# Kernel optimization log

Measured on AMD Instinct MI355X. Metric: run time of the kernel, lower is better.

## Reference

```python
import jax, jax.numpy as jnp
import numpy as np
from jax import lax

NUM_TAGS = 48
BATCH = 512
SEQ_LEN = 1024


def setup_inputs() -> dict:
    key = jax.random.key(0)
    k1, k2, k3, k4 = jax.random.split(key, 4)
    emissions = jax.random.normal(k1, (BATCH, SEQ_LEN, NUM_TAGS), dtype=jnp.float32)
    mask = jnp.ones((BATCH, SEQ_LEN), dtype=jnp.int32)
    transitions = jax.random.normal(k2, (NUM_TAGS, NUM_TAGS), dtype=jnp.float32)
    start_transitions = jax.random.normal(k3, (NUM_TAGS,), dtype=jnp.float32)
    end_transitions = jax.random.normal(k4, (NUM_TAGS,), dtype=jnp.float32)
    return {
        "emissions": emissions,
        "mask": mask,
        "transitions": transitions,
        "start_transitions": start_transitions,
        "end_transitions": end_transitions,
    }


def reference(emissions, mask, transitions, start_transitions, end_transitions):
    """Viterbi decode. mask is accepted but unused, matching the original module."""
    # emissions: [B, S, T]
    init_scores = start_transitions + emissions[:, 0]  # [B, T]

    def step(scores, em_t):
        # scores: [B, T] best score ending in each prev tag
        scores_with_trans = scores[:, :, None] + transitions  # [B, Tprev, Tcur]
        idx = jnp.argmax(scores_with_trans, axis=1)            # [B, T] backpointers
        new_scores = jnp.max(scores_with_trans, axis=1) + em_t  # [B, T]
        return new_scores, idx

    # scan over timesteps 1..S-1 (time-major emissions)
    em_rest = jnp.swapaxes(emissions[:, 1:], 0, 1)  # [S-1, B, T]
    scores, backptrs = lax.scan(step, init_scores, em_rest)  # backptrs: [S-1, B, T]

    scores = scores + end_transitions
    best_tags = jnp.argmax(scores, axis=1)  # [B] tag at position S-1

    def backtrace(tag, bp_t):
        # tag: [B] tag at position t+1; bp_t: [B, T] backpointers into position t
        prev = jnp.take_along_axis(bp_t, tag[:, None], axis=1)[:, 0]
        return prev, tag  # emit tag at position t+1

    first_tag, tags_rest = lax.scan(backtrace, best_tags, backptrs, reverse=True)
    # tags_rest[i] = tag at position i+1, shape [S-1, B]
    best_paths = jnp.concatenate(
        [first_tag[:, None], jnp.swapaxes(tags_rest, 0, 1)], axis=1
    )  # [B, S]
    return best_paths
```

## Files before the change

kernel.cpp:

```cpp
#include <hip/hip_runtime.h>

#define NTAG 48
#define SEQ 1024
#define NBATCH 512
#define NEG_INF (-3.402823466e+38f)

__device__ __forceinline__ float rl_f32(float v, int lane) {
    return __int_as_float(__builtin_amdgcn_readlane(__float_as_int(v), lane));
}

__device__ __forceinline__ float max3(float a, float b, float c) {
    float d;
    asm("v_max3_f32 %0, %1, %2, %3" : "=v"(d) : "v"(a), "v"(b), "v"(c));
    return d;
}

__global__ __launch_bounds__(64, 1) void crf_viterbi_kernel(
    const float* __restrict__ em,
    const float* __restrict__ trans,
    const float* __restrict__ start,
    const float* __restrict__ endt,
    int* __restrict__ out,
    float* __restrict__ srows)
{
    const int b  = blockIdx.x;
    const int j  = threadIdx.x;
    const int jj = (j < NTAG) ? j : (NTAG - 1);

    __shared__ float Ttr[NTAG * NTAG];
    __shared__ int obuf[SEQ];

#pragma unroll
    for (int k = 0; k < (NTAG * NTAG + 63) / 64; ++k) {
        int idx = k * 64 + j;
        if (idx < NTAG * NTAG) {
            int i = idx / NTAG, c = idx % NTAG;
            Ttr[c * NTAG + i] = trans[idx];
        }
    }

    float trg[NTAG];
#pragma unroll
    for (int i = 0; i < NTAG; ++i) trg[i] = trans[i * NTAG + jj];

    const float* emb = em + (size_t)b * SEQ * NTAG;
    float* srb = srows + (size_t)b * SEQ * NTAG;

    float score = start[jj] + emb[jj];
    if (j < NTAG) srb[j] = score;

    float em_p1 = emb[1 * NTAG + jj];
    float em_p2 = emb[2 * NTAG + jj];

    for (int t = 1; t < SEQ; ++t) {
        float em_j = em_p1;
        em_p1 = em_p2;
        int tn = (t + 2 < SEQ) ? (t + 2) : (SEQ - 1);
        em_p2 = emb[tn * NTAG + jj];

        float l1[16];
#pragma unroll
        for (int k = 0; k < 16; ++k) {
            float c0 = rl_f32(score, 3 * k)     + trg[3 * k];
            float c1 = rl_f32(score, 3 * k + 1) + trg[3 * k + 1];
            float c2 = rl_f32(score, 3 * k + 2) + trg[3 * k + 2];
            l1[k] = max3(c0, c1, c2);
        }
        float l2[6];
        l2[0] = max3(l1[0],  l1[1],  l1[2]);
        l2[1] = max3(l1[3],  l1[4],  l1[5]);
        l2[2] = max3(l1[6],  l1[7],  l1[8]);
        l2[3] = max3(l1[9],  l1[10], l1[11]);
        l2[4] = max3(l1[12], l1[13], l1[14]);
        l2[5] = l1[15];
        float m0 = max3(l2[0], l2[1], l2[2]);
        float m1 = max3(l2[3], l2[4], l2[5]);
        float best = fmaxf(m0, m1);

        score = best + em_j;
        if (j < NTAG) srb[(size_t)t * NTAG + j] = score;
    }

    float fs = (j < NTAG) ? (score + endt[jj]) : NEG_INF;
    float mx = fs;
    mx = fmaxf(mx, __shfl_xor(mx, 32, 64));
    mx = fmaxf(mx, __shfl_xor(mx, 16, 64));
    mx = fmaxf(mx, __shfl_xor(mx,  8, 64));
    mx = fmaxf(mx, __shfl_xor(mx,  4, 64));
    mx = fmaxf(mx, __shfl_xor(mx,  2, 64));
    mx = fmaxf(mx, __shfl_xor(mx,  1, 64));
    unsigned long long bl = __ballot(fs == mx);
    int jt = __ffsll(bl) - 1;

    if (j == 0) obuf[SEQ - 1] = jt;
    __syncthreads();

    float cur[8], nxt[8];
    int r = SEQ - 2;
#pragma unroll
    for (int k = 0; k < 8; ++k)
        cur[k] = srb[(size_t)(r - k) * NTAG + jj];

    int t = SEQ - 1;
    while (t >= 1) {
        int n = (t >= 8) ? 8 : t;
        int r2 = r - 8;
#pragma unroll
        for (int k = 0; k < 8; ++k)
            if (r2 - k >= 0) nxt[k] = srb[(size_t)(r2 - k) * NTAG + jj];

#pragma unroll
        for (int k = 0; k < 8; ++k) {
            if (k < n) {
                float tv = Ttr[jt * NTAG + jj];
                float v  = (j < NTAG) ? (cur[k] + tv) : NEG_INF;
                float m  = v;
                m = fmaxf(m, __shfl_xor(m, 32, 64));
                m = fmaxf(m, __shfl_xor(m, 16, 64));
                m = fmaxf(m, __shfl_xor(m,  8, 64));
                m = fmaxf(m, __shfl_xor(m,  4, 64));
                m = fmaxf(m, __shfl_xor(m,  2, 64));
                m = fmaxf(m, __shfl_xor(m,  1, 64));
                unsigned long long b2 = __ballot(v == m);
                jt = __ffsll(b2) - 1;
                if (j == 0) obuf[t - 1 - k] = jt;
            }
        }
        t -= n; r -= 8;
#pragma unroll
        for (int k = 0; k < 8; ++k) cur[k] = nxt[k];
    }

    __syncthreads();

    int* outb = out + (size_t)b * SEQ;
#pragma unroll
    for (int t0 = 0; t0 < SEQ / 64; ++t0)
        outb[t0 * 64 + j] = obuf[t0 * 64 + j];
}

extern "C" void kernel_launch(void* const* d_in, const int* in_sizes, int n_in,
                              void* d_out, int out_size, void* d_ws, size_t ws_size,
                              hipStream_t stream) {
    const float* em    = (const float*)d_in[0];
    const float* trans = (const float*)d_in[2];
    const float* start = (const float*)d_in[3];
    const float* endt  = (const float*)d_in[4];
    int* out = (int*)d_out;
    float* srows = (float*)d_ws;

    crf_viterbi_kernel<<<NBATCH, 64, 0, stream>>>(em, trans, start, endt, out, srows);
}
```

Before: 973.4 us.

## Stage emissions and score rows through double-buffered LDS via async global_load_lds

Emissions for 128-step chunks are copied into a double-buffered LDS stage with global_load_lds, replacing per-step global register prefetch in the forward pass. The backtrace likewise streams saved score rows from workspace into LDS chunks instead of per-row register prefetch. The aim is to take global memory latency off the serial per-step critical path. In exchange it adds 48KB of LDS and full vmcnt waits per chunk. The backtrace also reads rows just written by global stores, which relies on memory ordering for those stores.

```diff
diff --git a/kernel.cpp b/kernel.cpp
--- a/kernel.cpp
+++ b/kernel.cpp
@@ -3,6 +3,10 @@
 #define NTAG 48
 #define SEQ 1024
 #define NBATCH 512
+#define CH 128
+#define NCH (SEQ / CH)
+#define CHF (CH * NTAG)
+#define NISS (CHF * 4 / 1024)
 #define NEG_INF (-3.402823466e+38f)
 
 __device__ __forceinline__ float rl_f32(float v, int lane) {
@@ -14,6 +18,11 @@
     asm("v_max3_f32 %0, %1, %2, %3" : "=v"(d) : "v"(a), "v"(b), "v"(c));
     return d;
 }
+
+#define GLDS16(gp, lp)                                                                   \
+    __builtin_amdgcn_global_load_lds((const __attribute__((address_space(1))) void*)(gp),\
+                                     (__attribute__((address_space(3))) void*)(lp),      \
+                                     16, 0, 0)
 
 __global__ __launch_bounds__(64, 1) void crf_viterbi_kernel(
     const float* __restrict__ em,
@@ -27,6 +36,7 @@
     const int j  = threadIdx.x;
     const int jj = (j < NTAG) ? j : (NTAG - 1);
 
+    __shared__ float stage[2][CHF];
     __shared__ float Ttr[NTAG * NTAG];
     __shared__ int obuf[SEQ];
 
@@ -46,39 +56,51 @@
     const float* emb = em + (size_t)b * SEQ * NTAG;
     float* srb = srows + (size_t)b * SEQ * NTAG;
 
-    float score = start[jj] + emb[jj];
+#pragma unroll
+    for (int k = 0; k < NISS; ++k)
+        GLDS16(emb + k * 256 + j * 4, &stage[0][k * 256]);
+    asm volatile("s_waitcnt vmcnt(0)" ::: "memory");
+
+    float score = start[jj] + stage[0][jj];
     if (j < NTAG) srb[j] = score;
 
-    float em_p1 = emb[1 * NTAG + jj];
-    float em_p2 = emb[2 * NTAG + jj];
+    int cb = 0;
+    for (int c = 0; c < NCH; ++c) {
+        if (c + 1 < NCH) {
+            const float* gs = emb + (size_t)(c + 1) * CHF;
+#pragma unroll
+            for (int k = 0; k < NISS; ++k)
+                GLDS16(gs + k * 256 + j * 4, &stage[cb ^ 1][k * 256]);
+        }
+        const int tt0 = (c == 0) ? 1 : 0;
+        for (int tt = tt0; tt < CH; ++tt) {
+            float em_j = stage[cb][tt * NTAG + jj];
 
-    for (int t = 1; t < SEQ; ++t) {
-        float em_j = em_p1;
-        em_p1 = em_p2;
-        int tn = (t + 2 < SEQ) ? (t + 2) : (SEQ - 1);
-        em_p2 = emb[tn * NTAG + jj];
+            float l1[16];
+#pragma unroll
+            for (int k = 0; k < 16; ++k) {
+                float c0 = rl_f32(score, 3 * k)     + trg[3 * k];
+                float c1 = rl_f32(score, 3 * k + 1) + trg[3 * k + 1];
+                float c2 = rl_f32(score, 3 * k + 2) + trg[3 * k + 2];
+                l1[k] = max3(c0, c1, c2);
+            }
+            float l2[6];
+            l2[0] = max3(l1[0],  l1[1],  l1[2]);
+            l2[1] = max3(l1[3],  l1[4],  l1[5]);
+            l2[2] = max3(l1[6],  l1[7],  l1[8]);
+            l2[3] = max3(l1[9],  l1[10], l1[11]);
+            l2[4] = max3(l1[12], l1[13], l1[14]);
+            l2[5] = l1[15];
+            float m0 = max3(l2[0], l2[1], l2[2]);
+            float m1 = max3(l2[3], l2[4], l2[5]);
+            float best = fmaxf(m0, m1);
 
-        float l1[16];
-#pragma unroll
-        for (int k = 0; k < 16; ++k) {
-            float c0 = rl_f32(score, 3 * k)     + trg[3 * k];
-            float c1 = rl_f32(score, 3 * k + 1) + trg[3 * k + 1];
-            float c2 = rl_f32(score, 3 * k + 2) + trg[3 * k + 2];
-            l1[k] = max3(c0, c1, c2);
+            score = best + em_j;
+            int t = c * CH + tt;
+            if (j < NTAG) srb[(size_t)t * NTAG + j] = score;
         }
-        float l2[6];
-        l2[0] = max3(l1[0],  l1[1],  l1[2]);
-        l2[1] = max3(l1[3],  l1[4],  l1[5]);
-        l2[2] = max3(l1[6],  l1[7],  l1[8]);
-        l2[3] = max3(l1[9],  l1[10], l1[11]);
-        l2[4] = max3(l1[12], l1[13], l1[14]);
-        l2[5] = l1[15];
-        float m0 = max3(l2[0], l2[1], l2[2]);
-        float m1 = max3(l2[3], l2[4], l2[5]);
-        float best = fmaxf(m0, m1);
-
-        score = best + em_j;
-        if (j < NTAG) srb[(size_t)t * NTAG + j] = score;
+        asm volatile("s_waitcnt vmcnt(0)" ::: "memory");
+        cb ^= 1;
     }
 
     float fs = (j < NTAG) ? (score + endt[jj]) : NEG_INF;
@@ -93,42 +115,43 @@
     int jt = __ffsll(bl) - 1;
 
     if (j == 0) obuf[SEQ - 1] = jt;
-    __syncthreads();
 
-    float cur[8], nxt[8];
-    int r = SEQ - 2;
+    cb = 0;
+    {
+        const float* gs = srb + (size_t)(NCH - 1) * CHF;
 #pragma unroll
-    for (int k = 0; k < 8; ++k)
-        cur[k] = srb[(size_t)(r - k) * NTAG + jj];
+        for (int k = 0; k < NISS; ++k)
+            GLDS16(gs + k * 256 + j * 4, &stage[0][k * 256]);
+    }
+    asm volatile("s_waitcnt vmcnt(0)" ::: "memory");
 
-    int t = SEQ - 1;
-    while (t >= 1) {
-        int n = (t >= 8) ? 8 : t;
-        int r2 = r - 8;
+    for (int rc = NCH - 1; rc >= 0; --rc) {
+        if (rc > 0) {
+            const float* gs = srb + (size_t)(rc - 1) * CHF;
 #pragma unroll
-        for (int k = 0; k < 8; ++k)
-            if (r2 - k >= 0) nxt[k] = srb[(size_t)(r2 - k) * NTAG + jj];
-
-#pragma unroll
-        for (int k = 0; k < 8; ++k) {
-            if (k < n) {
-                float tv = Ttr[jt * NTAG + jj];
-                float v  = (j < NTAG) ? (cur[k] + tv) : NEG_INF;
-                float m  = v;
-                m = fmaxf(m, __shfl_xor(m, 32, 64));
-                m = fmaxf(m, __shfl_xor(m, 16, 64));
-                m = fmaxf(m, __shfl_xor(m,  8, 64));
-                m = fmaxf(m, __shfl_xor(m,  4, 64));
-                m = fmaxf(m, __shfl_xor(m,  2, 64));
-                m = fmaxf(m, __shfl_xor(m,  1, 64));
-                unsigned long long b2 = __ballot(v == m);
-                jt = __ffsll(b2) - 1;
-                if (j == 0) obuf[t - 1 - k] = jt;
-            }
+            for (int k = 0; k < NISS; ++k)
+                GLDS16(gs + k * 256 + j * 4, &stage[cb ^ 1][k * 256]);
         }
-        t -= n; r -= 8;
-#pragma unroll
-        for (int k = 0; k < 8; ++k) cur[k] = nxt[k];
+        const int thi = (rc == NCH - 1) ? (SEQ - 1) : (rc * CH + CH);
+        const int tlo = rc * CH + 1;
+        for (int t = thi; t >= tlo; --t) {
+            int lr = (t - 1) - rc * CH;
+            float sv = stage[cb][lr * NTAG + jj];
+            float tv = Ttr[jt * NTAG + jj];
+            float v  = (j < NTAG) ? (sv + tv) : NEG_INF;
+            float m  = v;
+            m = fmaxf(m, __shfl_xor(m, 32, 64));
+            m = fmaxf(m, __shfl_xor(m, 16, 64));
+            m = fmaxf(m, __shfl_xor(m,  8, 64));
+            m = fmaxf(m, __shfl_xor(m,  4, 64));
+            m = fmaxf(m, __shfl_xor(m,  2, 64));
+            m = fmaxf(m, __shfl_xor(m,  1, 64));
+            unsigned long long b2 = __ballot(v == m);
+            jt = __ffsll(b2) - 1;
+            if (j == 0) obuf[t - 1] = jt;
+        }
+        asm volatile("s_waitcnt vmcnt(0)" ::: "memory");
+        cb ^= 1;
     }
 
     __syncthreads();
```

Result: faster. 828.7 us (-14.9%).
